# Kernel tuning notes

Hardware: AMD Instinct MI355X
Metric: run time of the kernel (lower is better)

The kernel has to match this reference:

```python
import jax, jax.numpy as jnp
import numpy as np

L = 3
NC = (L + 1) ** 2                                   # 16 spherical components l=0..3
SO3_SIZES = [(2 * l + 1) ** 2 for l in range(L + 1)]  # [1,9,25,49]
SO3_OFF = np.cumsum([0] + SO3_SIZES).tolist()         # [0,1,10,35,84]
D3 = SO3_OFF[-1]                                      # 84 = dim of SO(3) signal irreps
MUL_SIZES = [2 * l + 1 for l in range(L + 1)]         # [1,3,5,7]
MUL_OFF = np.cumsum([0] + MUL_SIZES).tolist()         # [0,1,4,9,16]
LIDX = jnp.array(sum([[l] * (2 * l + 1) for l in range(L + 1)], []))  # comp -> l map (16,)
B, NPG = 32, 256
N = B * NPG
E = 32768
F = 16
MAXR = 3.5
NG = 4096


def real_sh(v):
    # component-normalized real spherical harmonics l=0..3 for unit vectors v (...,3)
    x, y, z = v[..., 0], v[..., 1], v[..., 2]
    s3, s5, s15 = 3.0 ** 0.5, 5.0 ** 0.5, 15.0 ** 0.5
    c = [jnp.ones_like(x),
         s3 * y, s3 * z, s3 * x,
         s15 * x * y, s15 * y * z, 0.5 * s5 * (3 * z * z - 1.0), s15 * x * z, 0.5 * s15 * (x * x - y * y),
         (35.0 / 8.0) ** 0.5 * y * (3 * x * x - y * y),
         105.0 ** 0.5 * x * y * z,
         (21.0 / 8.0) ** 0.5 * y * (5 * z * z - 1.0),
         0.5 * 7.0 ** 0.5 * (5 * z ** 3 - 3 * z),
         (21.0 / 8.0) ** 0.5 * x * (5 * z * z - 1.0),
         0.5 * 105.0 ** 0.5 * (x * x - y * y) * z,
         (35.0 / 8.0) ** 0.5 * x * (x * x - 3 * y * y)]
    return jnp.stack(c, axis=-1)


def gate(h):
    # equivariant gate: relu on l=0 scalars, sigmoid(scalar)-gated l>0 components
    s = h[..., 0:1]
    return jnp.concatenate([jax.nn.relu(s), h[..., 1:] * jax.nn.sigmoid(s)], axis=-1)


def setup_inputs() -> dict:
    key = jax.random.key(0)
    ks = jax.random.split(key, 16)
    rn = lambda k, s, sc=1.0: jax.random.normal(k, s, dtype=jnp.float32) * sc
    return {
        'node_feat': rn(ks[0], (N, F)),
        'pos': rn(ks[1], (N, 3), 1.5),
        'orientation': jax.random.uniform(ks[2], (B, 2), dtype=jnp.float32) * jnp.pi,
        'rad1_W1': rn(ks[3], (1, 64)),
        'rad1_b': jnp.zeros((64,), jnp.float32),
        'rad1_W2': rn(ks[4], (64, 2048), 0.1),
        'rad2_W1': rn(ks[5], (1, 64)),
        'rad2_b': jnp.zeros((64,), jnp.float32),
        'rad2_W2': rn(ks[6], (64, 2176), 0.1),
        'Wlin': rn(ks[7], (2 * F, F, NC)),
        'psi1': rn(ks[8], (16, 64, D3)),
        'psi2': rn(ks[9], (64, 128, D3)),
        'psi3': rn(ks[10], (128, 256, D3)),
        'G_to': rn(ks[11], (D3, NG)),
        'G_from': rn(ks[12], (NG, D3)),
        'Ws2': rn(ks[13], (256, 1, NC)),
        'edge_src': jax.random.randint(ks[14], (E,), 0, N, dtype=jnp.int32),
        'edge_dst': jax.random.randint(ks[15], (E,), 0, N, dtype=jnp.int32),
        'batch': jnp.repeat(jnp.arange(B, dtype=jnp.int32), NPG),
    }


def reference(node_feat, pos, orientation, rad1_W1, rad1_b, rad1_W2, rad2_W1, rad2_b,
              rad2_W2, Wlin, psi1, psi2, psi3, G_to, G_from, Ws2,
              edge_src, edge_dst, batch):
    # ---- encoder: radius-graph equivariant message passing (gather / TP / scatter) ----
    ev = pos[edge_dst] - pos[edge_src]
    d = jnp.linalg.norm(ev, axis=-1) + 1e-9
    Y = real_sh(ev / d[:, None])                              # (E,16) edge SH
    u = d / MAXR
    cut = jnp.where(u < 1.0, 0.5 * (jnp.cos(jnp.pi * u) + 1.0), 0.0)

    def radial(W1, b, W2):
        hh = jax.nn.relu(u[:, None] * W1 + b)                 # (E,64)
        return (hh @ W2) * cut[:, None]

    deg = (E / N) ** 0.5
    # layer 1: scalar-in x SH tensor product with per-edge radial weights
    w1 = radial(rad1_W1, rad1_b, rad1_W2).reshape(E, F, F, 2, L + 1)
    t1 = jnp.einsum('ef,efgpl->egpl', node_feat[edge_src], w1) / (F ** 0.5)
    msg1 = t1[:, :, :, LIDX] * Y[:, None, None, :]            # (E,16,2,16)
    h1 = jax.ops.segment_sum(msg1, edge_dst, num_segments=N) / deg
    h1 = gate(h1)
    # layer 2: scalar x SH path + l_in (x) 0e self path
    w2 = radial(rad2_W1, rad2_b, rad2_W2)
    w2sh = w2[:, :2048].reshape(E, F, F, 2, L + 1)
    w2self = w2[:, 2048:].reshape(E, F, 2, L + 1)
    t2 = jnp.einsum('ef,efgpl->egpl', h1[:, :, 0, 0][edge_src], w2sh) / (F ** 0.5)
    msg2 = t2[:, :, :, LIDX] * Y[:, None, None, :] + h1[edge_src] * w2self[:, :, :, LIDX]
    h2 = jax.ops.segment_sum(msg2, edge_dst, num_segments=N) / deg
    h2 = gate(h2)
    # mean-pool readout per graph -> (B, 512)
    cnt = jax.ops.segment_sum(jnp.ones((N,), h2.dtype), batch, num_segments=B)
    enc = jax.ops.segment_sum(h2.reshape(N, -1), batch, num_segments=B) / cnt[:, None]

    # ---- o3.Linear enc_out -> so3_irreps latent z (B, F, 84) ----
    e = enc.reshape(B, 2 * F, NC)
    zs = []
    for l in range(L + 1):
        c0, c1 = MUL_OFF[l], MUL_OFF[l + 1]
        zl = jnp.einsum('bmc,mgj->bgjc', e[:, :, c0:c1], Wlin[:, :, c0:c1]) / (2 * F) ** 0.5
        zs.append(zl.reshape(B, F, -1))
    z = jnp.concatenate(zs, axis=-1)

    # ---- decoder: SO(3) equivariant convs + grid activations ----
    def so3_conv(x, psi):
        fi, fo = psi.shape[0], psi.shape[1]
        outs = []
        for l in range(L + 1):
            o0, o1 = SO3_OFF[l], SO3_OFF[l + 1]
            m = 2 * l + 1
            xl = x[:, :, o0:o1].reshape(B, fi, m, m)
            pl = psi[:, :, o0:o1].reshape(fi, fo, m, m)
            ol = jnp.einsum('bfic,fgij->bgjc', xl, pl) / (fi * m) ** 0.5
            outs.append(ol.reshape(B, fo, m * m))
        return jnp.concatenate(outs, axis=-1)

    def so3_act(x):
        g = jax.nn.relu(jnp.einsum('bfd,dg->bfg', x, G_to) / D3 ** 0.5)
        return jnp.einsum('bfg,gd->bfd', g, G_from) / NG ** 0.5

    x = so3_act(so3_conv(z, psi1))
    x = so3_act(so3_conv(x, psi2))
    x = so3_act(so3_conv(x, psi3))

    # ---- SO3 -> S2 convolution -> (B, out_dim, 16) ----
    outs = []
    for l in range(L + 1):
        o0, o1 = SO3_OFF[l], SO3_OFF[l + 1]
        m = 2 * l + 1
        xl = x[:, :, o0:o1].reshape(B, 256, m, m)
        Wl = Ws2[:, :, MUL_OFF[l]:MUL_OFF[l + 1]]
        outs.append(jnp.einsum('bfic,fgi->bgc', xl, Wl) / (256 * m) ** 0.5)
    s2 = jnp.concatenate(outs, axis=-1)

    # ---- aspect/roll -> cartesian line-of-sight -> SH response (bmm) ----
    a, r = orientation[..., 0], orientation[..., 1]
    cart = jnp.stack([-jnp.sin(a) * jnp.cos(r), -jnp.sin(a) * jnp.sin(r), -jnp.cos(a)], axis=-1)
    shp = real_sh(cart)                                       # (B,16)
    return jnp.einsum('bgc,bc->bg', s2, shp)[:, 0]            # (B,)
```

## Files before the change

### kernel.cpp

```cpp
#include <hip/hip_runtime.h>
#include <math.h>

#define DEV static __device__ __forceinline__

constexpr int NN = 8192;
constexpr int NE = 32768;
constexpr int NB = 32;

using short8 = __attribute__((ext_vector_type(8))) short;
using half8  = __attribute__((ext_vector_type(8))) _Float16;
using f32x4  = __attribute__((ext_vector_type(4))) float;

DEV ushort f2bf(float f) {
  unsigned u = __float_as_uint(f);
  unsigned r = (u + 0x7FFFu + ((u >> 16) & 1u)) >> 16;
  return (ushort)r;
}
DEV float bf2f(ushort h) { return __uint_as_float(((unsigned)h) << 16); }

DEV void split8h(const float* p, half8& hi, half8& lo) {
#pragma unroll
  for (int j = 0; j < 8; ++j) {
    const _Float16 h = (_Float16)p[j];
    hi[j] = h;
    lo[j] = (_Float16)(p[j] - (float)h);
  }
}

DEV int lidx_of(int c) { return (c == 0) ? 0 : (c < 4) ? 1 : (c < 9) ? 2 : 3; }

DEV void real_sh_f(float x, float y, float z, float* Y) {
  const float s3  = 1.7320508075688772f;
  const float s5  = 2.23606797749979f;
  const float s15 = 3.872983346207417f;
  Y[0] = 1.f;
  Y[1] = s3 * y;  Y[2] = s3 * z;  Y[3] = s3 * x;
  Y[4] = s15 * x * y;
  Y[5] = s15 * y * z;
  Y[6] = 0.5f * s5 * (3.f * z * z - 1.f);
  Y[7] = s15 * x * z;
  Y[8] = 0.5f * s15 * (x * x - y * y);
  Y[9]  = 2.091650066335189f * y * (3.f * x * x - y * y);
  Y[10] = 10.246950765959598f * x * y * z;
  Y[11] = 1.6201851746019651f * y * (5.f * z * z - 1.f);
  Y[12] = 1.3228756555322954f * (5.f * z * z * z - 3.f * z);
  Y[13] = 1.6201851746019651f * x * (5.f * z * z - 1.f);
  Y[14] = 5.123475382979799f * (x * x - y * y) * z;
  Y[15] = 2.091650066335189f * x * (x * x - 3.f * y * y);
}

__global__ __launch_bounds__(256) void k_edge_prep(
    const float* __restrict__ pos, const int* __restrict__ esrc,
    const int* __restrict__ edst, float* __restrict__ u_, float* __restrict__ cut_,
    float* __restrict__ Y_, int* __restrict__ cnt) {
  const int e = blockIdx.x * 256 + threadIdx.x;
  if (e >= NE) return;
  const int s = esrc[e], t = edst[e];
  const float ex = pos[t * 3 + 0] - pos[s * 3 + 0];
  const float ey = pos[t * 3 + 1] - pos[s * 3 + 1];
  const float ez = pos[t * 3 + 2] - pos[s * 3 + 2];
  const float d = sqrtf(ex * ex + ey * ey + ez * ez) + 1e-9f;
  const float inv = 1.f / d;
  float Y[16];
  real_sh_f(ex * inv, ey * inv, ez * inv, Y);
#pragma unroll
  for (int c = 0; c < 16; ++c) Y_[(size_t)e * 16 + c] = Y[c];
  const float u = d / 3.5f;
  u_[e] = u;
  cut_[e] = (u < 1.f) ? 0.5f * (cosf(3.14159265358979323846f * u) + 1.f) : 0.f;
  atomicAdd(&cnt[t], 1);
}

__global__ __launch_bounds__(256) void k_scan(const int* __restrict__ cnt,
                                              int* __restrict__ offs,
                                              int* __restrict__ cursor) {
  __shared__ int part[256];
  const int t = threadIdx.x;
  int s = 0;
  for (int i = 0; i < 32; ++i) s += cnt[t * 32 + i];
  part[t] = s;
  __syncthreads();
  if (t == 0) {
    int run = 0;
    for (int i = 0; i < 256; ++i) { int v = part[i]; part[i] = run; run += v; }
    offs[NN] = run;
  }
  __syncthreads();
  int run = part[t];
  for (int i = 0; i < 32; ++i) {
    const int idx = t * 32 + i;
    offs[idx] = run;
    cursor[idx] = run;
    run += cnt[idx];
  }
}

__global__ __launch_bounds__(256) void k_fill(const int* __restrict__ edst,
                                              int* __restrict__ cursor,
                                              int* __restrict__ elist) {
  const int e = blockIdx.x * 256 + threadIdx.x;
  if (e < NE) {
    const int p = atomicAdd(&cursor[edst[e]], 1);
    elist[p] = e;
  }
}

template <bool IS2>
__global__ __launch_bounds__(256) void k_prep_w2t(const float* __restrict__ W2,
                                                  ushort* __restrict__ Th,
                                                  ushort* __restrict__ Tl) {
  const int idx = blockIdx.x * 256 + threadIdx.x;
  if (idx >= 128 * 1024) return;
  const int o = idx >> 10, kf = idx & 1023;
  const float v = IS2 ? W2[(size_t)(kf >> 4) * 2176 + (kf & 15) * 128 + o]
                      : W2[(size_t)kf * 128 + o];
  const _Float16 h = (_Float16)v;
  ((_Float16*)Th)[idx] = h;
  ((_Float16*)Tl)[idx] = (_Float16)(v - (float)h);
}

__global__ __launch_bounds__(256) void k_prep_selfw(const float* __restrict__ W2,
                                                    ushort* __restrict__ Sh,
                                                    ushort* __restrict__ Sl) {
  const int idx = blockIdx.x * 256 + threadIdx.x;
  if (idx >= 128 * 64) return;
  const int o = idx >> 6, k = idx & 63;
  const float v = W2[(size_t)k * 2176 + 2048 + o];
  const _Float16 h = (_Float16)v;
  ((_Float16*)Sh)[idx] = h;
  ((_Float16*)Sl)[idx] = (_Float16)(v - (float)h);
}

#define MSG_STEP(HS, BH, BL)                                                     \
  do {                                                                           \
    half8 ah_[4], al_[4];                                                        \
    _Pragma("unroll") for (int mt = 0; mt < 4; ++mt) {                           \
      float p_[8];                                                               \
      _Pragma("unroll") for (int j = 0; j < 8; ++j) p_[j] = HS[mt] * nf8[mt][j]; \
      split8h(p_, ah_[mt], al_[mt]);                                             \
    }                                                                            \
    _Pragma("unroll") for (int n = 0; n < 2; ++n) {                              \
      _Pragma("unroll") for (int mt = 0; mt < 4; ++mt) {                         \
        acc[mt][n] = __builtin_amdgcn_mfma_f32_16x16x32_f16(ah_[mt], BH[n], acc[mt][n], 0, 0, 0); \
        acc[mt][n] = __builtin_amdgcn_mfma_f32_16x16x32_f16(al_[mt], BH[n], acc[mt][n], 0, 0, 0); \
        acc[mt][n] = __builtin_amdgcn_mfma_f32_16x16x32_f16(ah_[mt], BL[n], acc[mt][n], 0, 0, 0); \
      }                                                                          \
    }                                                                            \
  } while (0)

template <bool IS2>
__global__ __launch_bounds__(256) void k_msg_mfma(
    const float* __restrict__ u_, const float* __restrict__ cut_,
    const float* __restrict__ W1, const float* __restrict__ bvec,
    const ushort* __restrict__ W2Th, const ushort* __restrict__ W2Tl,
    const ushort* __restrict__ SWh, const ushort* __restrict__ SWl,
    const float* __restrict__ feat16, const int* __restrict__ esrc,
    float* __restrict__ t_, float* __restrict__ self_) {
  __shared__ float hhL[64 * 65];
  __shared__ float nfL[64 * 17];
  __shared__ float uL[64], cL[64];
  __shared__ int sL[64];
  const int tid = threadIdx.x;
  const int e0 = blockIdx.x * 64;
  if (tid < 64) {
    uL[tid] = u_[e0 + tid];
    cL[tid] = cut_[e0 + tid];
    sL[tid] = esrc[e0 + tid];
  }
  __syncthreads();
  for (int i = tid; i < 64 * 64; i += 256) {
    const int e = i >> 6, k = i & 63;
    hhL[e * 65 + k] = fmaxf(fmaf(uL[e], W1[k], bvec[k]), 0.f) * cL[e];
  }
  for (int i = tid; i < 64 * 16; i += 256) {
    const int e = i >> 4, f = i & 15;
    nfL[e * 17 + f] = feat16[(size_t)sL[e] * 16 + f];
  }
  __syncthreads();

  const int lane = tid & 63, wv = tid >> 6;
  const int lr = lane & 15, lg = lane >> 4;
  const int n0 = wv * 2;

  if (IS2) {
    f32x4 sacc[4][2];
#pragma unroll
    for (int mt = 0; mt < 4; ++mt)
#pragma unroll
      for (int n = 0; n < 2; ++n) {
        f32x4 zz = {0.f, 0.f, 0.f, 0.f};
        sacc[mt][n] = zz;
      }
#pragma unroll
    for (int ks2 = 0; ks2 < 2; ++ks2) {
      half8 ash[4], asl[4];
#pragma unroll
      for (int mt = 0; mt < 4; ++mt) {
        float p[8];
        const float* hp = &hhL[(mt * 16 + lr) * 65 + ks2 * 32 + lg * 8];
#pragma unroll
        for (int j = 0; j < 8; ++j) p[j] = hp[j];
        split8h(p, ash[mt], asl[mt]);
      }
#pragma unroll
      for (int n = 0; n < 2; ++n) {
        const half8 bh = *(const half8*)&SWh[((n0 + n) * 16 + lr) * 64 + ks2 * 32 + lg * 8];
        const half8 bl = *(const half8*)&SWl[((n0 + n) * 16 + lr) * 64 + ks2 * 32 + lg * 8];
#pragma unroll
        for (int mt = 0; mt < 4; ++mt) {
          sacc[mt][n] = __builtin_amdgcn_mfma_f32_16x16x32_f16(ash[mt], bh, sacc[mt][n], 0, 0, 0);
          sacc[mt][n] = __builtin_amdgcn_mfma_f32_16x16x32_f16(asl[mt], bh, sacc[mt][n], 0, 0, 0);
          sacc[mt][n] = __builtin_amdgcn_mfma_f32_16x16x32_f16(ash[mt], bl, sacc[mt][n], 0, 0, 0);
        }
      }
    }
#pragma unroll
    for (int mt = 0; mt < 4; ++mt)
#pragma unroll
      for (int n = 0; n < 2; ++n)
#pragma unroll
        for (int i = 0; i < 4; ++i)
          self_[(size_t)(e0 + mt * 16 + lg * 4 + i) * 128 + (n0 + n) * 16 + lr] =
              sacc[mt][n][i] * 0.5f;
  }

  float nf8[4][8];
#pragma unroll
  for (int mt = 0; mt < 4; ++mt)
#pragma unroll
    for (int j = 0; j < 8; ++j)
      nf8[mt][j] = nfL[(mt * 16 + lr) * 17 + (lg & 1) * 8 + j];

  f32x4 acc[4][2];
#pragma unroll
  for (int mt = 0; mt < 4; ++mt)
#pragma unroll
    for (int n = 0; n < 2; ++n) {
      f32x4 zz = {0.f, 0.f, 0.f, 0.f};
      acc[mt][n] = zz;
    }

  const ushort* bh_base[2] = {
    &W2Th[(size_t)((n0 + 0) * 16 + lr) * 1024 + lg * 8],
    &W2Th[(size_t)((n0 + 1) * 16 + lr) * 1024 + lg * 8]};
  const ushort* bl_base[2] = {
    &W2Tl[(size_t)((n0 + 0) * 16 + lr) * 1024 + lg * 8],
    &W2Tl[(size_t)((n0 + 1) * 16 + lr) * 1024 + lg * 8]};
  const float* hs_base[4] = {&hhL[(0 * 16 + lr) * 65 + (lg >> 1)],
                             &hhL[(1 * 16 + lr) * 65 + (lg >> 1)],
                             &hhL[(2 * 16 + lr) * 65 + (lg >> 1)],
                             &hhL[(3 * 16 + lr) * 65 + (lg >> 1)]};

  half8 bhA[2], blA[2], bhB[2], blB[2];
  float hsA[4], hsB[4];
#pragma unroll
  for (int n = 0; n < 2; ++n) {
    bhA[n] = *(const half8*)(bh_base[n]);
    blA[n] = *(const half8*)(bl_base[n]);
  }
#pragma unroll
  for (int mt = 0; mt < 4; ++mt) hsA[mt] = hs_base[mt][0];

  for (int ks = 0; ks < 32; ks += 2) {
#pragma unroll
    for (int n = 0; n < 2; ++n) {
      bhB[n] = *(const half8*)(bh_base[n] + (ks + 1) * 32);
      blB[n] = *(const half8*)(bl_base[n] + (ks + 1) * 32);
    }
#pragma unroll
    for (int mt = 0; mt < 4; ++mt) hsB[mt] = hs_base[mt][2 * (ks + 1)];
    MSG_STEP(hsA, bhA, blA);
    if (ks + 2 < 32) {
#pragma unroll
      for (int n = 0; n < 2; ++n) {
        bhA[n] = *(const half8*)(bh_base[n] + (ks + 2) * 32);
        blA[n] = *(const half8*)(bl_base[n] + (ks + 2) * 32);
      }
#pragma unroll
      for (int mt = 0; mt < 4; ++mt) hsA[mt] = hs_base[mt][2 * (ks + 2)];
    }
    MSG_STEP(hsB, bhB, blB);
  }
#pragma unroll
  for (int mt = 0; mt < 4; ++mt)
#pragma unroll
    for (int n = 0; n < 2; ++n)
#pragma unroll
      for (int i = 0; i < 4; ++i)
        t_[(size_t)(e0 + mt * 16 + lg * 4 + i) * 128 + (n0 + n) * 16 + lr] =
            acc[mt][n][i] * 0.125f;
}

__global__ __launch_bounds__(256) void k_gather1(
    const float* __restrict__ t_, const float* __restrict__ Y_,
    const int* __restrict__ offs, const int* __restrict__ elist,
    float* __restrict__ h1, float* __restrict__ h1s) {
  __shared__ float tL[128], YL[16], sG[32];
  const int n = blockIdx.x, tid = threadIdx.x;
  const int beg = offs[n], end = offs[n + 1];
  const int cc = tid & 15;
  const int lx = lidx_of(cc);
  const int o0 = ((tid >> 4) << 2) + lx;
  const int o1 = o0 + 64;
  float a0 = 0.f, a1 = 0.f;
  for (int ei = beg; ei < end; ++ei) {
    const int e = elist[ei];
    __syncthreads();
    if (tid < 128) tL[tid] = t_[(size_t)e * 128 + tid];
    else if (tid < 144) YL[tid - 128] = Y_[(size_t)e * 16 + tid - 128];
    __syncthreads();
    const float yv = YL[cc];
    a0 = fmaf(tL[o0], yv, a0);
    a1 = fmaf(tL[o1], yv, a1);
  }
  if (cc == 0) { sG[tid >> 4] = a0; sG[(tid >> 4) + 16] = a1; }
  __syncthreads();
  const float s0 = sG[tid >> 4], s1 = sG[(tid >> 4) + 16];
  const float r0 = (cc == 0) ? fmaxf(a0, 0.f) : a0 * (1.f / (1.f + expf(-s0)));
  const float r1 = (cc == 0) ? fmaxf(a1, 0.f) : a1 * (1.f / (1.f + expf(-s1)));
  h1[(size_t)n * 512 + tid] = r0;
  h1[(size_t)n * 512 + tid + 256] = r1;
  if ((tid & 31) == 0) {
    h1s[n * 16 + (tid >> 5)] = r0;
    h1s[n * 16 + (tid >> 5) + 8] = r1;
  }
}

__global__ __launch_bounds__(256) void k_gather2(
    const float* __restrict__ t_, const float* __restrict__ self_,
    const float* __restrict__ Y_, const float* __restrict__ h1,
    const int* __restrict__ offs, const int* __restrict__ elist,
    const int* __restrict__ esrc, float* __restrict__ h2) {
  __shared__ float tL[128], wL[128], YL[16], sG[32];
  const int n = blockIdx.x, tid = threadIdx.x;
  const int beg = offs[n], end = offs[n + 1];
  const int cc = tid & 15;
  const int lx = lidx_of(cc);
  const int o0 = ((tid >> 4) << 2) + lx;
  const int o1 = o0 + 64;
  float a0 = 0.f, a1 = 0.f;
  for (int ei = beg; ei < end; ++ei) {
    const int e = elist[ei];
    __syncthreads();
    if (tid < 128) tL[tid] = t_[(size_t)e * 128 + tid];
    else wL[tid - 128] = self_[(size_t)e * 128 + tid - 128];
    if (tid < 16) YL[tid] = Y_[(size_t)e * 16 + tid];
    __syncthreads();
    const int src = esrc[e];
    const float* hr = &h1[(size_t)src * 512];
    const float yv = YL[cc];
    a0 += tL[o0] * yv + hr[tid] * wL[o0];
    a1 += tL[o1] * yv + hr[tid + 256] * wL[o1];
  }
  if (cc == 0) { sG[tid >> 4] = a0; sG[(tid >> 4) + 16] = a1; }
  __syncthreads();
  const float s0 = sG[tid >> 4], s1 = sG[(tid >> 4) + 16];
  const float r0 = (cc == 0) ? fmaxf(a0, 0.f) : a0 * (1.f / (1.f + expf(-s0)));
  const float r1 = (cc == 0) ? fmaxf(a1, 0.f) : a1 * (1.f / (1.f + expf(-s1)));
  h2[(size_t)n * 512 + tid] = r0;
  h2[(size_t)n * 512 + tid + 256] = r1;
}

__global__ __launch_bounds__(256) void k_pool(const float* __restrict__ h2,
                                              float* __restrict__ enc) {
  const int b = blockIdx.x, tid = threadIdx.x;
  float a0 = 0.f, a1 = 0.f;
  for (int i = 0; i < 256; ++i) {
    const float* row = &h2[(size_t)(b * 256 + i) * 512];
    a0 += row[tid];
    a1 += row[tid + 256];
  }
  enc[b * 512 + tid] = a0 * (1.f / 256.f);
  enc[b * 512 + tid + 256] = a1 * (1.f / 256.f);
}

__global__ __launch_bounds__(256) void k_zproj(const float* __restrict__ enc,
                                               const float* __restrict__ Wlin,
                                               float* __restrict__ z) {
  __shared__ float eL[512];
  const int b = blockIdx.x, tid = threadIdx.x;
  eL[tid] = enc[b * 512 + tid];
  eL[tid + 256] = enc[b * 512 + tid + 256];
  __syncthreads();
  for (int idx = tid; idx < 16 * 84; idx += 256) {
    const int g = idx / 84, d3 = idx % 84;
    int o0, m0, mo;
    if (d3 < 1)       { o0 = 0;  m0 = 1; mo = 0; }
    else if (d3 < 10) { o0 = 1;  m0 = 3; mo = 1; }
    else if (d3 < 35) { o0 = 10; m0 = 5; mo = 4; }
    else              { o0 = 35; m0 = 7; mo = 9; }
    const int rem = d3 - o0;
    const int jj = rem / m0;
    const int cc2 = rem - jj * m0;
    float a = 0.f;
    for (int mu = 0; mu < 32; ++mu)
      a = fmaf(eL[mu * 16 + mo + cc2], Wlin[(mu * 16 + g) * 16 + mo + jj], a);
    z[(size_t)(b * 16 + g) * 84 + d3] = a * 0.17677669529663687f;
  }
}

template <int FI>
__global__ __launch_bounds__(256) void k_prep_xg(const float* __restrict__ x,
                                                 ushort* __restrict__ Xh,
                                                 ushort* __restrict__ Xl) {
  constexpr int KP0 = (FI + 31) & ~31, KP1 = (3 * FI + 31) & ~31;
  constexpr int KP2 = (5 * FI + 31) & ~31, KP3 = (7 * FI + 31) & ~31;
  constexpr int XO1 = 32 * KP0, XO2 = XO1 + 96 * KP1, XO3 = XO2 + 160 * KP2;
  constexpr int TOT = XO3 + 224 * KP3;
  const int idx = blockIdx.x * 256 + threadIdx.x;
  if (idx >= TOT) return;
  int m, o0, base, KP;
  if (idx < XO1)      { m = 1; o0 = 0;  base = 0;   KP = KP0; }
  else if (idx < XO2) { m = 3; o0 = 1;  base = XO1; KP = KP1; }
  else if (idx < XO3) { m = 5; o0 = 10; base = XO2; KP = KP2; }
  else                { m = 7; o0 = 35; base = XO3; KP = KP3; }
  const int rel = idx - base;
  const int r = rel / KP, k = rel % KP;
  ushort h = 0, lo = 0;
  if (k < FI * m) {
    const int f = k / m, i = k % m, b = r / m, c = r % m;
    const float v = x[((size_t)b * FI + f) * 84 + o0 + i * m + c];
    h = f2bf(v);
    lo = (ushort)(__float_as_uint(v - bf2f(h)) >> 16);
  }
  Xh[idx] = h;
  Xl[idx] = lo;
}

template <int FI, int FO>
__global__ __launch_bounds__(256) void k_prep_psig(const float* __restrict__ psi,
                                                   ushort* __restrict__ Ph,
                                                   ushort* __restrict__ Pl) {
  constexpr int KP0 = (FI + 31) & ~31, KP1 = (3 * FI + 31) & ~31;
  constexpr int KP2 = (5 * FI + 31) & ~31, KP3 = (7 * FI + 31) & ~31;
  constexpr int PO1 = FO * KP0, PO2 = PO1 + 3 * FO * KP1, PO3 = PO2 + 5 * FO * KP2;
  constexpr int TOT = PO3 + 7 * FO * KP3;
  const int idx = blockIdx.x * 256 + threadIdx.x;
  if (idx >= TOT) return;
  int m, o0, base, KP;
  if (idx < PO1)      { m = 1; o0 = 0;  base = 0;   KP = KP0; }
  else if (idx < PO2) { m = 3; o0 = 1;  base = PO1; KP = KP1; }
  else if (idx < PO3) { m = 5; o0 = 10; base = PO2; KP = KP2; }
  else                { m = 7; o0 = 35; base = PO3; KP = KP3; }
  const int rel = idx - base;
  const int n = rel / KP, k = rel % KP;
  ushort h = 0, lo = 0;
  if (k < FI * m) {
    const int f = k / m, i = k % m, g = n / m, j = n % m;
    const float v = psi[((size_t)f * FO + g) * 84 + o0 + i * m + j];
    h = f2bf(v);
    lo = (ushort)(__float_as_uint(v - bf2f(h)) >> 16);
  }
  Ph[idx] = h;
  Pl[idx] = lo;
}

template <int FI, int FO>
__global__ __launch_bounds__(256) void k_conv_gemm(
    const ushort* __restrict__ Xh, const ushort* __restrict__ Xl,
    const ushort* __restrict__ Ph, const ushort* __restrict__ Pl,
    float* __restrict__ out) {
  constexpr int KP0 = (FI + 31) & ~31, KP1 = (3 * FI + 31) & ~31;
  constexpr int KP2 = (5 * FI + 31) & ~31, KP3 = (7 * FI + 31) & ~31;
  constexpr int XO1 = 32 * KP0, XO2 = XO1 + 96 * KP1, XO3 = XO2 + 160 * KP2;
  constexpr int PO1 = FO * KP0, PO2 = PO1 + 3 * FO * KP1, PO3 = PO2 + 5 * FO * KP2;
  constexpr int NT0 = 1 * (FO / 32), NT1 = 3 * (3 * FO / 32);
  constexpr int NT2 = 5 * (5 * FO / 32), NT3 = 7 * (7 * FO / 32);
  constexpr int TB1 = NT0, TB2 = TB1 + NT1, TB3 = TB2 + NT2, TOT = TB3 + NT3;

  const int wt = blockIdx.x * 4 + (threadIdx.x >> 6);
  if (wt >= TOT) return;
  int m, o0, Mt, KP, Xo, Po, loc;
  if (wt < TB1)      { m = 1; o0 = 0;  Mt = 1; KP = KP0; Xo = 0;   Po = 0;   loc = wt; }
  else if (wt < TB2) { m = 3; o0 = 1;  Mt = 3; KP = KP1; Xo = XO1; Po = PO1; loc = wt - TB1; }
  else if (wt < TB3) { m = 5; o0 = 10; Mt = 5; KP = KP2; Xo = XO2; Po = PO2; loc = wt - TB2; }
  else               { m = 7; o0 = 35; Mt = 7; KP = KP3; Xo = XO3; Po = PO3; loc = wt - TB3; }
  const int mt0 = (loc % Mt) * 32;
  const int nt0 = (loc / Mt) * 32;
  const int lane = threadIdx.x & 63, lr = lane & 15, lg = lane >> 4;

  f32x4 acc[2][2];
#pragma unroll
  for (int mt = 0; mt < 2; ++mt)
#pragma unroll
    for (int nt = 0; nt < 2; ++nt) {
      f32x4 zz = {0.f, 0.f, 0.f, 0.f};
      acc[mt][nt] = zz;
    }

  const int nks = KP >> 5;
  for (int ks = 0; ks < nks; ++ks) {
    short8 ah[2], al[2], bh[2], bl[2];
#pragma unroll
    for (int t = 0; t < 2; ++t) {
      const size_t xa = (size_t)Xo + (size_t)(mt0 + t * 16 + lr) * KP + ks * 32 + lg * 8;
      ah[t] = *(const short8*)&Xh[xa];
      al[t] = *(const short8*)&Xl[xa];
      const size_t pa = (size_t)Po + (size_t)(nt0 + t * 16 + lr) * KP + ks * 32 + lg * 8;
      bh[t] = *(const short8*)&Ph[pa];
      bl[t] = *(const short8*)&Pl[pa];
    }
#pragma unroll
    for (int nt = 0; nt < 2; ++nt)
#pragma unroll
      for (int mt = 0; mt < 2; ++mt) {
        acc[mt][nt] = __builtin_amdgcn_mfma_f32_16x16x32_bf16(ah[mt], bh[nt], acc[mt][nt], 0, 0, 0);
        acc[mt][nt] = __builtin_amdgcn_mfma_f32_16x16x32_bf16(al[mt], bh[nt], acc[mt][nt], 0, 0, 0);
        acc[mt][nt] = __builtin_amdgcn_mfma_f32_16x16x32_bf16(ah[mt], bl[nt], acc[mt][nt], 0, 0, 0);
      }
  }

  const float scale = 1.f / sqrtf((float)(FI * m));
#pragma unroll
  for (int mt = 0; mt < 2; ++mt)
#pragma unroll
    for (int nt = 0; nt < 2; ++nt)
#pragma unroll
      for (int i = 0; i < 4; ++i) {
        const int R = mt0 + mt * 16 + lg * 4 + i;
        const int C2 = nt0 + nt * 16 + lr;
        const int b = R / m, c = R - b * m;
        const int g = C2 / m, j = C2 - g * m;
        out[((size_t)b * FO + g) * 84 + o0 + j * m + c] = acc[mt][nt][i] * scale;
      }
}

__global__ __launch_bounds__(256) void k_prep_gt(const float* __restrict__ Gt,
                                                 ushort* __restrict__ GtT) {
  const int idx = blockIdx.x * 256 + threadIdx.x;
  if (idx >= 4096 * 96) return;
  const int g = idx / 96, k = idx % 96;
  GtT[idx] = (k < 84) ? f2bf(Gt[(size_t)k * 4096 + g]) : (ushort)0;
}
__global__ __launch_bounds__(256) void k_prep_gf(const float* __restrict__ Gf,
                                                 ushort* __restrict__ GfT) {
  const int idx = blockIdx.x * 256 + threadIdx.x;
  if (idx >= 96 * 4096) return;
  const int d = idx / 4096, g = idx % 4096;
  GfT[idx] = (d < 84) ? f2bf(Gf[(size_t)g * 84 + d]) : (ushort)0;
}
__global__ __launch_bounds__(256) void k_cvtx(const float* __restrict__ x,
                                              ushort* __restrict__ Xb, int total) {
  const int idx = blockIdx.x * 256 + threadIdx.x;
  if (idx >= total) return;
  const int r = idx / 96, k = idx % 96;
  Xb[idx] = (k < 84) ? f2bf(x[(size_t)r * 84 + k]) : (ushort)0;
}

template <int GS>
__global__ __launch_bounds__(256) void k_act_mfma(
    const ushort* __restrict__ Xb, const ushort* __restrict__ GtT,
    const ushort* __restrict__ GfT, float* __restrict__ part, int NR) {
  constexpr int CPB = 64 / GS;
  __shared__ __align__(16) ushort ldsGt[64 * 104];
  __shared__ __align__(16) ushort ldsH[128 * 72];
  __shared__ __align__(16) ushort ldsGf[96 * 72];
  const int tid = threadIdx.x;
  const int gs = blockIdx.x;
  const int row0 = blockIdx.y * 128;
  const int lane = tid & 63, wv = tid >> 6;
  const int lr = lane & 15, lg = lane >> 4;
  const int m0 = wv * 32;

  short8 a1[2][3];
#pragma unroll
  for (int mt = 0; mt < 2; ++mt)
#pragma unroll
    for (int ks = 0; ks < 3; ++ks)
      a1[mt][ks] = *(const short8*)&Xb[(size_t)(row0 + m0 + mt * 16 + lr) * 96 +
                                       ks * 32 + lg * 8];

  f32x4 acc2[6][2];
#pragma unroll
  for (int m2 = 0; m2 < 6; ++m2)
#pragma unroll
    for (int n2 = 0; n2 < 2; ++n2) {
      f32x4 zz = {0.f, 0.f, 0.f, 0.f};
      acc2[m2][n2] = zz;
    }

  for (int ch = gs * CPB; ch < (gs + 1) * CPB; ++ch) {
    const int g0 = ch * 64;
    __syncthreads();
    for (int i = tid; i < 768; i += 256) {
      const int row = i / 12, c = i % 12;
      *(uint4*)&ldsGt[row * 104 + c * 8] =
          *(const uint4*)&GtT[(size_t)(g0 + row) * 96 + c * 8];
    }
    for (int i = tid; i < 768; i += 256) {
      const int row = i / 8, c = i % 8;
      *(uint4*)&ldsGf[row * 72 + c * 8] =
          *(const uint4*)&GfT[(size_t)row * 4096 + g0 + c * 8];
    }
    __syncthreads();
#pragma unroll
    for (int n = 0; n < 4; ++n) {
      short8 b[3];
#pragma unroll
      for (int ks = 0; ks < 3; ++ks)
        b[ks] = *(const short8*)&ldsGt[(n * 16 + lr) * 104 + ks * 32 + lg * 8];
#pragma unroll
      for (int mt = 0; mt < 2; ++mt) {
        f32x4 c1 = {0.f, 0.f, 0.f, 0.f};
#pragma unroll
        for (int ks = 0; ks < 3; ++ks)
          c1 = __builtin_amdgcn_mfma_f32_16x16x32_bf16(a1[mt][ks], b[ks], c1, 0, 0, 0);
        ushort* hp = &ldsH[(m0 + mt * 16 + lg * 4) * 72 + n * 16 + lr];
#pragma unroll
        for (int i = 0; i < 4; ++i) hp[i * 72] = f2bf(fmaxf(c1[i], 0.f));
      }
    }
#pragma unroll
    for (int k2 = 0; k2 < 2; ++k2) {
      short8 bh[2];
#pragma unroll
      for (int n2 = 0; n2 < 2; ++n2)
        bh[n2] = *(const short8*)&ldsH[(m0 + n2 * 16 + lr) * 72 + k2 * 32 + lg * 8];
#pragma unroll
      for (int m2 = 0; m2 < 6; ++m2) {
        const short8 a2 = *(const short8*)&ldsGf[(m2 * 16 + lr) * 72 + k2 * 32 + lg * 8];
        acc2[m2][0] = __builtin_amdgcn_mfma_f32_16x16x32_bf16(a2, bh[0], acc2[m2][0], 0, 0, 0);
        acc2[m2][1] = __builtin_amdgcn_mfma_f32_16x16x32_bf16(a2, bh[1], acc2[m2][1], 0, 0, 0);
      }
    }
  }
#pragma unroll
  for (int m2 = 0; m2 < 6; ++m2)
#pragma unroll
    for (int n2 = 0; n2 < 2; ++n2)
#pragma unroll
      for (int i = 0; i < 4; ++i) {
        const int d = m2 * 16 + lg * 4 + i;
        if (d < 84) {
          const int r = row0 + m0 + n2 * 16 + lr;
          part[((size_t)gs * NR + r) * 84 + d] = acc2[m2][n2][i];
        }
      }
}

template <int GS>
__global__ __launch_bounds__(256) void k_act_reduce(const float* __restrict__ part,
                                                    float* __restrict__ out, int total) {
  const int i = blockIdx.x * 256 + threadIdx.x;
  if (i < total) {
    float s = part[i];
#pragma unroll
    for (int g = 1; g < GS; ++g) s += part[(size_t)g * total + i];
    out[i] = s * (1.f / (9.16515138991168f * 64.f));
  }
}

__global__ __launch_bounds__(256) void k_final(const float* __restrict__ x,
                                               const float* __restrict__ Ws2,
                                               const float* __restrict__ orient,
                                               float* __restrict__ outp) {
  __shared__ float red[256][16];
  const int b = blockIdx.x, tid = threadIdx.x;
  const float* xr = &x[(size_t)(b * 256 + tid) * 84];
  const float* wr = &Ws2[tid * 16];
  float acc[16];
#pragma unroll
  for (int c = 0; c < 16; ++c) acc[c] = 0.f;
  acc[0] = fmaf(xr[0], wr[0], acc[0]);
#pragma unroll
  for (int i = 0; i < 3; ++i) {
    const float w = wr[1 + i];
#pragma unroll
    for (int c = 0; c < 3; ++c) acc[1 + c] = fmaf(xr[1 + i * 3 + c], w, acc[1 + c]);
  }
#pragma unroll
  for (int i = 0; i < 5; ++i) {
    const float w = wr[4 + i];
#pragma unroll
    for (int c = 0; c < 5; ++c) acc[4 + c] = fmaf(xr[10 + i * 5 + c], w, acc[4 + c]);
  }
#pragma unroll
  for (int i = 0; i < 7; ++i) {
    const float w = wr[9 + i];
#pragma unroll
    for (int c = 0; c < 7; ++c) acc[9 + c] = fmaf(xr[35 + i * 7 + c], w, acc[9 + c]);
  }
#pragma unroll
  for (int c = 0; c < 16; ++c) red[tid][c] = acc[c];
  __syncthreads();
  for (int off = 128; off > 0; off >>= 1) {
    if (tid < off)
#pragma unroll
      for (int c = 0; c < 16; ++c) red[tid][c] += red[tid + off][c];
    __syncthreads();
  }
  if (tid == 0) {
    const float aa = orient[b * 2 + 0], rr = orient[b * 2 + 1];
    float Y[16];
    real_sh_f(-sinf(aa) * cosf(rr), -sinf(aa) * sinf(rr), -cosf(aa), Y);
    const float sc1 = 1.f / 16.f;
    const float sc3 = 1.f / (16.f * 1.7320508075688772f);
    const float sc5 = 1.f / (16.f * 2.23606797749979f);
    const float sc7 = 1.f / (16.f * 2.6457513110645907f);
    float o = red[0][0] * sc1 * Y[0];
#pragma unroll
    for (int c = 1; c < 4; ++c) o += red[0][c] * sc3 * Y[c];
#pragma unroll
    for (int c = 4; c < 9; ++c) o += red[0][c] * sc5 * Y[c];
#pragma unroll
    for (int c = 9; c < 16; ++c) o += red[0][c] * sc7 * Y[c];
    outp[b] = o;
  }
}

extern "C" void kernel_launch(void* const* d_in, const int* in_sizes, int n_in,
                              void* d_out, int out_size, void* d_ws, size_t ws_size,
                              hipStream_t stream) {
  const float* node_feat = (const float*)d_in[0];
  const float* pos       = (const float*)d_in[1];
  const float* orient    = (const float*)d_in[2];
  const float* rad1_W1   = (const float*)d_in[3];
  const float* rad1_b    = (const float*)d_in[4];
  const float* rad1_W2   = (const float*)d_in[5];
  const float* rad2_W1   = (const float*)d_in[6];
  const float* rad2_b    = (const float*)d_in[7];
  const float* rad2_W2   = (const float*)d_in[8];
  const float* Wlin      = (const float*)d_in[9];
  const float* psi1      = (const float*)d_in[10];
  const float* psi2      = (const float*)d_in[11];
  const float* psi3      = (const float*)d_in[12];
  const float* G_to      = (const float*)d_in[13];
  const float* G_from    = (const float*)d_in[14];
  const float* Ws2       = (const float*)d_in[15];
  const int*   esrc      = (const int*)d_in[16];
  const int*   edst      = (const int*)d_in[17];

  float* w = (float*)d_ws;
  size_t off = 0;
  float* u_    = w + off; off += NE;
  float* cut_  = w + off; off += NE;
  float* Y_    = w + off; off += (size_t)NE * 16;
  float* t_    = w + off; off += (size_t)NE * 128;
  float* self_ = w + off; off += (size_t)NE * 128;
  float* h1    = w + off; off += (size_t)NN * 512;
  float* h1s   = w + off; off += (size_t)NN * 16;
  float* h2    = w + off; off += (size_t)NN * 512;
  float* enc   = w + off; off += (size_t)NB * 512;
  float* z     = w + off; off += (size_t)NB * 16 * 84;
  float* xb1   = w + off; off += (size_t)NB * 256 * 84;
  float* xb2   = w + off; off += (size_t)NB * 256 * 84;
  int* cnt    = (int*)(w + off); off += NN;
  int* offs   = (int*)(w + off); off += NN + 1;
  int* cursor = (int*)(w + off); off += NN;
  int* elist  = (int*)(w + off); off += NE;
  ushort* W2Th = (ushort*)(w + off); off += 65536;
  ushort* W2Tl = (ushort*)(w + off); off += 65536;
  ushort* SWh  = (ushort*)(w + off); off += 4096;
  ushort* SWl  = (ushort*)(w + off); off += 4096;

  float* part = t_;
  ushort* GtT = (ushort*)h1;
  ushort* GfT = GtT + 4096 * 96;
  ushort* Xb  = GfT + 96 * 4096;
  ushort* Xph = (ushort*)Y_;
  ushort* Xpl = Xph + 344064;
  ushort* Pph = (ushort*)h2;
  ushort* Ppl = Pph + 2752512;

  hipMemsetAsync(cnt, 0, NN * sizeof(int), stream);
  k_edge_prep<<<NE / 256, 256, 0, stream>>>(pos, esrc, edst, u_, cut_, Y_, cnt);
  k_scan<<<1, 256, 0, stream>>>(cnt, offs, cursor);
  k_fill<<<NE / 256, 256, 0, stream>>>(edst, cursor, elist);

  k_prep_w2t<false><<<512, 256, 0, stream>>>(rad1_W2, W2Th, W2Tl);
  k_msg_mfma<false><<<NE / 64, 256, 0, stream>>>(u_, cut_, rad1_W1, rad1_b, W2Th, W2Tl,
                                                 nullptr, nullptr, node_feat, esrc,
                                                 t_, nullptr);
  k_gather1<<<NN, 256, 0, stream>>>(t_, Y_, offs, elist, h1, h1s);

  k_prep_w2t<true><<<512, 256, 0, stream>>>(rad2_W2, W2Th, W2Tl);
  k_prep_selfw<<<32, 256, 0, stream>>>(rad2_W2, SWh, SWl);
  k_msg_mfma<true><<<NE / 64, 256, 0, stream>>>(u_, cut_, rad2_W1, rad2_b, W2Th, W2Tl,
                                                SWh, SWl, h1s, esrc, t_, self_);
  k_gather2<<<NN, 256, 0, stream>>>(t_, self_, Y_, h1, offs, elist, esrc, h2);
  k_pool<<<NB, 256, 0, stream>>>(h2, enc);
  k_zproj<<<NB, 256, 0, stream>>>(enc, Wlin, z);

  k_prep_gt<<<(4096 * 96 + 255) / 256, 256, 0, stream>>>(G_to, GtT);
  k_prep_gf<<<(96 * 4096 + 255) / 256, 256, 0, stream>>>(G_from, GfT);

  k_prep_psig<16, 64><<<(102400 + 255) / 256, 256, 0, stream>>>(psi1, Pph, Ppl);
  k_prep_xg<16><<<(51200 + 255) / 256, 256, 0, stream>>>(z, Xph, Xpl);
  k_conv_gemm<16, 64><<<42, 256, 0, stream>>>(Xph, Xpl, Pph, Ppl, xb1);
  k_cvtx<<<(2048 * 96 + 255) / 256, 256, 0, stream>>>(xb1, Xb, 2048 * 96);
  k_act_mfma<32><<<dim3(32, 16), 256, 0, stream>>>(Xb, GtT, GfT, part, 2048);
  k_act_reduce<32><<<(2048 * 84 + 255) / 256, 256, 0, stream>>>(part, xb2, 2048 * 84);

  k_prep_psig<64, 128><<<(688128 + 255) / 256, 256, 0, stream>>>(psi2, Pph, Ppl);
  k_prep_xg<64><<<(172032 + 255) / 256, 256, 0, stream>>>(xb2, Xph, Xpl);
  k_conv_gemm<64, 128><<<84, 256, 0, stream>>>(Xph, Xpl, Pph, Ppl, xb1);
  k_cvtx<<<(4096 * 96 + 255) / 256, 256, 0, stream>>>(xb1, Xb, 4096 * 96);
  k_act_mfma<16><<<dim3(16, 32), 256, 0, stream>>>(Xb, GtT, GfT, part, 4096);
  k_act_reduce<16><<<(4096 * 84 + 255) / 256, 256, 0, stream>>>(part, xb2, 4096 * 84);

  k_prep_psig<128, 256><<<(2752512 + 255) / 256, 256, 0, stream>>>(psi3, Pph, Ppl);
  k_prep_xg<128><<<(344064 + 255) / 256, 256, 0, stream>>>(xb2, Xph, Xpl);
  k_conv_gemm<128, 256><<<168, 256, 0, stream>>>(Xph, Xpl, Pph, Ppl, xb1);
  k_cvtx<<<(8192 * 96 + 255) / 256, 256, 0, stream>>>(xb1, Xb, 8192 * 96);
  k_act_mfma<8><<<dim3(8, 64), 256, 0, stream>>>(Xb, GtT, GfT, part, 8192);
  k_act_reduce<8><<<(8192 * 84 + 255) / 256, 256, 0, stream>>>(part, xb2, 8192 * 84);

  k_final<<<NB, 256, 0, stream>>>(xb2, Ws2, orient, (float*)d_out);
}
```

Measured before the change: 383.2 us.

## Split message GEMM K-loop across two wave groups; one wave per node in gathers

The message-passing MFMA kernel now runs 512 threads per block. Two groups of four waves each handle half of the K dimension, and their partial accumulators are reduced through shared memory before the store. The node gather kernels switch from one 256-thread block per node with block-wide barriers to one wave per node, using only wave barriers, with four nodes per block. The aim is more latency-hiding parallelism in the GEMM and fewer costly __syncthreads per edge in the gathers. The trade-off is higher register and LDS pressure per block and a serial four-item loop per lane in the gathers.

```diff
diff --git a/kernel.cpp b/kernel.cpp
--- a/kernel.cpp
+++ b/kernel.cpp
@@ -149,17 +149,19 @@
   } while (0)
 
 template <bool IS2>
-__global__ __launch_bounds__(256) void k_msg_mfma(
+__global__ __launch_bounds__(512) void k_msg_mfma(
     const float* __restrict__ u_, const float* __restrict__ cut_,
     const float* __restrict__ W1, const float* __restrict__ bvec,
     const ushort* __restrict__ W2Th, const ushort* __restrict__ W2Tl,
     const ushort* __restrict__ SWh, const ushort* __restrict__ SWl,
     const float* __restrict__ feat16, const int* __restrict__ esrc,
     float* __restrict__ t_, float* __restrict__ self_) {
-  __shared__ float hhL[64 * 65];
-  __shared__ float nfL[64 * 17];
-  __shared__ float uL[64], cL[64];
-  __shared__ int sL[64];
+  __shared__ float smem[8448];
+  float* uL  = smem;
+  float* cL  = smem + 64;
+  int*   sL  = (int*)(smem + 128);
+  float* hhL = smem + 192;
+  float* nfL = smem + 4352;
   const int tid = threadIdx.x;
   const int e0 = blockIdx.x * 64;
   if (tid < 64) {
@@ -168,21 +170,22 @@
     sL[tid] = esrc[e0 + tid];
   }
   __syncthreads();
-  for (int i = tid; i < 64 * 64; i += 256) {
+  for (int i = tid; i < 64 * 64; i += 512) {
     const int e = i >> 6, k = i & 63;
     hhL[e * 65 + k] = fmaxf(fmaf(uL[e], W1[k], bvec[k]), 0.f) * cL[e];
   }
-  for (int i = tid; i < 64 * 16; i += 256) {
+  for (int i = tid; i < 64 * 16; i += 512) {
     const int e = i >> 4, f = i & 15;
     nfL[e * 17 + f] = feat16[(size_t)sL[e] * 16 + f];
   }
   __syncthreads();
 
   const int lane = tid & 63, wv = tid >> 6;
+  const int wq = wv & 3, kh = wv >> 2;
   const int lr = lane & 15, lg = lane >> 4;
-  const int n0 = wv * 2;
-
-  if (IS2) {
+  const int n0 = wq * 2;
+
+  if (IS2 && kh == 0) {
     f32x4 sacc[4][2];
 #pragma unroll
     for (int mt = 0; mt < 4; ++mt)
@@ -251,17 +254,18 @@
                              &hhL[(2 * 16 + lr) * 65 + (lg >> 1)],
                              &hhL[(3 * 16 + lr) * 65 + (lg >> 1)]};
 
+  const int ks0 = kh * 16, ks1 = ks0 + 16;
   half8 bhA[2], blA[2], bhB[2], blB[2];
   float hsA[4], hsB[4];
 #pragma unroll
   for (int n = 0; n < 2; ++n) {
-    bhA[n] = *(const half8*)(bh_base[n]);
-    blA[n] = *(const half8*)(bl_base[n]);
-  }
-#pragma unroll
-  for (int mt = 0; mt < 4; ++mt) hsA[mt] = hs_base[mt][0];
-
-  for (int ks = 0; ks < 32; ks += 2) {
+    bhA[n] = *(const half8*)(bh_base[n] + ks0 * 32);
+    blA[n] = *(const half8*)(bl_base[n] + ks0 * 32);
+  }
+#pragma unroll
+  for (int mt = 0; mt < 4; ++mt) hsA[mt] = hs_base[mt][2 * ks0];
+
+  for (int ks = ks0; ks < ks1; ks += 2) {
 #pragma unroll
     for (int n = 0; n < 2; ++n) {
       bhB[n] = *(const half8*)(bh_base[n] + (ks + 1) * 32);
@@ -270,7 +274,7 @@
 #pragma unroll
     for (int mt = 0; mt < 4; ++mt) hsB[mt] = hs_base[mt][2 * (ks + 1)];
     MSG_STEP(hsA, bhA, blA);
-    if (ks + 2 < 32) {
+    if (ks + 2 < ks1) {
 #pragma unroll
       for (int n = 0; n < 2; ++n) {
         bhA[n] = *(const half8*)(bh_base[n] + (ks + 2) * 32);
@@ -281,48 +285,91 @@
     }
     MSG_STEP(hsB, bhB, blB);
   }
-#pragma unroll
-  for (int mt = 0; mt < 4; ++mt)
-#pragma unroll
-    for (int n = 0; n < 2; ++n)
-#pragma unroll
-      for (int i = 0; i < 4; ++i)
-        t_[(size_t)(e0 + mt * 16 + lg * 4 + i) * 128 + (n0 + n) * 16 + lr] =
-            acc[mt][n][i] * 0.125f;
+
+  __syncthreads();
+  if (kh == 1) {
+#pragma unroll
+    for (int mt = 0; mt < 4; ++mt)
+#pragma unroll
+      for (int n = 0; n < 2; ++n)
+#pragma unroll
+        for (int i = 0; i < 4; ++i)
+          smem[wq * 2112 + lane * 33 + mt * 8 + n * 4 + i] = acc[mt][n][i];
+  }
+  __syncthreads();
+  if (kh == 0) {
+#pragma unroll
+    for (int mt = 0; mt < 4; ++mt)
+#pragma unroll
+      for (int n = 0; n < 2; ++n)
+#pragma unroll
+        for (int i = 0; i < 4; ++i) {
+          const float v = acc[mt][n][i] +
+                          smem[wq * 2112 + lane * 33 + mt * 8 + n * 4 + i];
+          t_[(size_t)(e0 + mt * 16 + lg * 4 + i) * 128 + (n0 + n) * 16 + lr] =
+              v * 0.125f;
+        }
+  }
 }
 
 __global__ __launch_bounds__(256) void k_gather1(
     const float* __restrict__ t_, const float* __restrict__ Y_,
     const int* __restrict__ offs, const int* __restrict__ elist,
     float* __restrict__ h1, float* __restrict__ h1s) {
-  __shared__ float tL[128], YL[16], sG[32];
-  const int n = blockIdx.x, tid = threadIdx.x;
+  __shared__ float lds[4 * 176];
+  const int tid = threadIdx.x, lane = tid & 63, wv = tid >> 6;
+  const int n = blockIdx.x * 4 + wv;
+  float* tW = &lds[wv * 176];
+  float* YW = tW + 128;
+  float* sW = tW + 144;
   const int beg = offs[n], end = offs[n + 1];
-  const int cc = tid & 15;
-  const int lx = lidx_of(cc);
-  const int o0 = ((tid >> 4) << 2) + lx;
-  const int o1 = o0 + 64;
-  float a0 = 0.f, a1 = 0.f;
+  int o0q[4], o1q[4], ccq[4];
+#pragma unroll
+  for (int q = 0; q < 4; ++q) {
+    const int tv = lane + 64 * q;
+    const int cc = tv & 15;
+    ccq[q] = cc;
+    o0q[q] = ((tv >> 4) << 2) + lidx_of(cc);
+    o1q[q] = o0q[q] + 64;
+  }
+  float a0[4] = {0.f, 0.f, 0.f, 0.f}, a1[4] = {0.f, 0.f, 0.f, 0.f};
   for (int ei = beg; ei < end; ++ei) {
     const int e = elist[ei];
-    __syncthreads();
-    if (tid < 128) tL[tid] = t_[(size_t)e * 128 + tid];
-    else if (tid < 144) YL[tid - 128] = Y_[(size_t)e * 16 + tid - 128];
-    __syncthreads();
-    const float yv = YL[cc];
-    a0 = fmaf(tL[o0], yv, a0);
-    a1 = fmaf(tL[o1], yv, a1);
-  }
-  if (cc == 0) { sG[tid >> 4] = a0; sG[(tid >> 4) + 16] = a1; }
-  __syncthreads();
-  const float s0 = sG[tid >> 4], s1 = sG[(tid >> 4) + 16];
-  const float r0 = (cc == 0) ? fmaxf(a0, 0.f) : a0 * (1.f / (1.f + expf(-s0)));
-  const float r1 = (cc == 0) ? fmaxf(a1, 0.f) : a1 * (1.f / (1.f + expf(-s1)));
-  h1[(size_t)n * 512 + tid] = r0;
-  h1[(size_t)n * 512 + tid + 256] = r1;
-  if ((tid & 31) == 0) {
-    h1s[n * 16 + (tid >> 5)] = r0;
-    h1s[n * 16 + (tid >> 5) + 8] = r1;
+    const float2 v = *(const float2*)&t_[(size_t)e * 128 + lane * 2];
+    tW[lane * 2] = v.x;
+    tW[lane * 2 + 1] = v.y;
+    if (lane < 16) YW[lane] = Y_[(size_t)e * 16 + lane];
+    __builtin_amdgcn_wave_barrier();
+#pragma unroll
+    for (int q = 0; q < 4; ++q) {
+      const float yv = YW[ccq[q]];
+      a0[q] = fmaf(tW[o0q[q]], yv, a0[q]);
+      a1[q] = fmaf(tW[o1q[q]], yv, a1[q]);
+    }
+    __builtin_amdgcn_wave_barrier();
+  }
+#pragma unroll
+  for (int q = 0; q < 4; ++q)
+    if (ccq[q] == 0) {
+      const int tv = lane + 64 * q;
+      sW[tv >> 4] = a0[q];
+      sW[(tv >> 4) + 16] = a1[q];
+    }
+  __builtin_amdgcn_wave_barrier();
+#pragma unroll
+  for (int q = 0; q < 4; ++q) {
+    const int tv = lane + 64 * q;
+    const float s0 = sW[tv >> 4], s1 = sW[(tv >> 4) + 16];
+    const float r0 = (ccq[q] == 0) ? fmaxf(a0[q], 0.f)
+                                   : a0[q] * (1.f / (1.f + expf(-s0)));
+    const float r1 = (ccq[q] == 0) ? fmaxf(a1[q], 0.f)
+                                   : a1[q] * (1.f / (1.f + expf(-s1)));
+    h1[(size_t)n * 512 + tv] = r0;
+    h1[(size_t)n * 512 + tv + 256] = r1;
+    if ((tv & 31) == 0) {
+      h1s[n * 16 + (tv >> 5)] = r0;
+      h1s[n * 16 + (tv >> 5) + 8] = r1;
+    }
   }
 }
 
@@ -331,34 +378,64 @@
     const float* __restrict__ Y_, const float* __restrict__ h1,
     const int* __restrict__ offs, const int* __restrict__ elist,
     const int* __restrict__ esrc, float* __restrict__ h2) {
-  __shared__ float tL[128], wL[128], YL[16], sG[32];
-  const int n = blockIdx.x, tid = threadIdx.x;
+  __shared__ float lds[4 * 304];
+  const int tid = threadIdx.x, lane = tid & 63, wv = tid >> 6;
+  const int n = blockIdx.x * 4 + wv;
+  float* tW = &lds[wv * 304];
+  float* wL = tW + 128;
+  float* YW = tW + 256;
+  float* sW = tW + 272;
   const int beg = offs[n], end = offs[n + 1];
-  const int cc = tid & 15;
-  const int lx = lidx_of(cc);
-  const int o0 = ((tid >> 4) << 2) + lx;
-  const int o1 = o0 + 64;
-  float a0 = 0.f, a1 = 0.f;
+  int o0q[4], o1q[4], ccq[4];
+#pragma unroll
+  for (int q = 0; q < 4; ++q) {
+    const int tv = lane + 64 * q;
+    const int cc = tv & 15;
+    ccq[q] = cc;
+    o0q[q] = ((tv >> 4) << 2) + lidx_of(cc);
+    o1q[q] = o0q[q] + 64;
+  }
+  float a0[4] = {0.f, 0.f, 0.f, 0.f}, a1[4] = {0.f, 0.f, 0.f, 0.f};
   for (int ei = beg; ei < end; ++ei) {
     const int e = elist[ei];
-    __syncthreads();
-    if (tid < 128) tL[tid] = t_[(size_t)e * 128 + tid];
-    else wL[tid - 128] = self_[(size_t)e * 128 + tid - 128];
-    if (tid < 16) YL[tid] = Y_[(size_t)e * 16 + tid];
-    __syncthreads();
+    const float2 v = *(const float2*)&t_[(size_t)e * 128 + lane * 2];
+    const float2 w2 = *(const float2*)&self_[(size_t)e * 128 + lane * 2];
+    tW[lane * 2] = v.x;
+    tW[lane * 2 + 1] = v.y;
+    wL[lane * 2] = w2.x;
+    wL[lane * 2 + 1] = w2.y;
+    if (lane < 16) YW[lane] = Y_[(size_t)e * 16 + lane];
+    __builtin_amdgcn_wave_barrier();
     const int src = esrc[e];
     const float* hr = &h1[(size_t)src * 512];
-    const float yv = YL[cc];
-    a0 += tL[o0] * yv + hr[tid] * wL[o0];
-    a1 += tL[o1] * yv + hr[tid + 256] * wL[o1];
-  }
-  if (cc == 0) { sG[tid >> 4] = a0; sG[(tid >> 4) + 16] = a1; }
-  __syncthreads();
-  const float s0 = sG[tid >> 4], s1 = sG[(tid >> 4) + 16];
-  const float r0 = (cc == 0) ? fmaxf(a0, 0.f) : a0 * (1.f / (1.f + expf(-s0)));
-  const float r1 = (cc == 0) ? fmaxf(a1, 0.f) : a1 * (1.f / (1.f + expf(-s1)));
-  h2[(size_t)n * 512 + tid] = r0;
-  h2[(size_t)n * 512 + tid + 256] = r1;
+#pragma unroll
+    for (int q = 0; q < 4; ++q) {
+      const int tv = lane + 64 * q;
+      const float yv = YW[ccq[q]];
+      a0[q] += tW[o0q[q]] * yv + hr[tv] * wL[o0q[q]];
+      a1[q] += tW[o1q[q]] * yv + hr[tv + 256] * wL[o1q[q]];
+    }
+    __builtin_amdgcn_wave_barrier();
+  }
+#pragma unroll
+  for (int q = 0; q < 4; ++q)
+    if (ccq[q] == 0) {
+      const int tv = lane + 64 * q;
+      sW[tv >> 4] = a0[q];
+      sW[(tv >> 4) + 16] = a1[q];
+    }
+  __builtin_amdgcn_wave_barrier();
+#pragma unroll
+  for (int q = 0; q < 4; ++q) {
+    const int tv = lane + 64 * q;
+    const float s0 = sW[tv >> 4], s1 = sW[(tv >> 4) + 16];
+    const float r0 = (ccq[q] == 0) ? fmaxf(a0[q], 0.f)
+                                   : a0[q] * (1.f / (1.f + expf(-s0)));
+    const float r1 = (ccq[q] == 0) ? fmaxf(a1[q], 0.f)
+                                   : a1[q] * (1.f / (1.f + expf(-s1)));
+    h2[(size_t)n * 512 + tv] = r0;
+    h2[(size_t)n * 512 + tv + 256] = r1;
+  }
 }
 
 __global__ __launch_bounds__(256) void k_pool(const float* __restrict__ h2,
@@ -446,8 +523,9 @@
   const int n = rel / KP, k = rel % KP;
   ushort h = 0, lo = 0;
   if (k < FI * m) {
-    const int f = k / m, i = k % m, g = n / m, j = n % m;
-    const float v = psi[((size_t)f * FO + g) * 84 + o0 + i * m + j];
+    const int f = k / m, i = k % m, g = n / KP0 * 0 + n / m, j = n % m;
+    const float v = psi[((size_t)f * FO + (n / m)) * 84 + o0 + i * m + j];
+    (void)g;
     h = f2bf(v);
     lo = (ushort)(__float_as_uint(v - bf2f(h)) >> 16);
   }
@@ -768,16 +846,16 @@
   k_fill<<<NE / 256, 256, 0, stream>>>(edst, cursor, elist);
 
   k_prep_w2t<false><<<512, 256, 0, stream>>>(rad1_W2, W2Th, W2Tl);
-  k_msg_mfma<false><<<NE / 64, 256, 0, stream>>>(u_, cut_, rad1_W1, rad1_b, W2Th, W2Tl,
+  k_msg_mfma<false><<<NE / 64, 512, 0, stream>>>(u_, cut_, rad1_W1, rad1_b, W2Th, W2Tl,
                                                  nullptr, nullptr, node_feat, esrc,
                                                  t_, nullptr);
-  k_gather1<<<NN, 256, 0, stream>>>(t_, Y_, offs, elist, h1, h1s);
+  k_gather1<<<NN / 4, 256, 0, stream>>>(t_, Y_, offs, elist, h1, h1s);
 
   k_prep_w2t<true><<<512, 256, 0, stream>>>(rad2_W2, W2Th, W2Tl);
   k_prep_selfw<<<32, 256, 0, stream>>>(rad2_W2, SWh, SWl);
-  k_msg_mfma<true><<<NE / 64, 256, 0, stream>>>(u_, cut_, rad2_W1, rad2_b, W2Th, W2Tl,
+  k_msg_mfma<true><<<NE / 64, 512, 0, stream>>>(u_, cut_, rad2_W1, rad2_b, W2Th, W2Tl,
                                                 SWh, SWl, h1s, esrc, t_, self_);
-  k_gather2<<<NN, 256, 0, stream>>>(t_, self_, Y_, h1, offs, elist, esrc, h2);
+  k_gather2<<<NN / 4, 256, 0, stream>>>(t_, self_, Y_, h1, offs, elist, esrc, h2);
   k_pool<<<NB, 256, 0, stream>>>(h2, enc);
   k_zproj<<<NB, 256, 0, stream>>>(enc, Wlin, z);
 
```

Measured after the change: 371.8 us. -3.0%, faster.
